# Kernel optimization log

Measured on AMD Instinct MI355X. Metric: run time of the kernel, lower is better.

Reference implementation:

```python
import jax, jax.numpy as jnp
import numpy as np

B, N, M, D, H = 2, 1024, 1024, 768, 72  # H = num_layers*nhead = 6*12

def setup_inputs() -> dict:
    key = jax.random.key(0)
    ks = jax.random.split(key, 7)
    s = lambda fan_in: 1.0 / np.sqrt(fan_in)
    return {
        "x": jax.random.normal(ks[0], (B, N, D), dtype=jnp.float32),
        "stacked_scores": jax.random.normal(ks[1], (B, H, N, M), dtype=jnp.float32),
        "W1": jax.random.uniform(ks[2], (D, D // 2), jnp.float32, -s(D), s(D)),
        "b1": jax.random.uniform(ks[3], (D // 2,), jnp.float32, -s(D), s(D)),
        "W2": jax.random.uniform(ks[4], (D // 2, H), jnp.float32, -s(D // 2), s(D // 2)),
        "b2": jax.random.uniform(ks[5], (H,), jnp.float32, -s(D // 2), s(D // 2)),
        "bias": jnp.zeros((1,), dtype=jnp.float32),
    }

def reference(x, stacked_scores, W1, b1, W2, b2, bias):
    # Router MLP: Linear -> exact GELU -> Linear  => raw_weights [b, n, h]
    h = jax.nn.gelu(jnp.einsum('bnd,df->bnf', x, W1) + b1, approximate=False)
    raw_weights = jnp.einsum('bnf,fh->bnh', h, W2) + b2
    # Weighted combine of stacked attention maps, reducing over heads
    final_matrix = jnp.einsum('bnh,bhnm->bnm', raw_weights, stacked_scores)
    return final_matrix + bias
```

## Files before the change

kernel.cpp:

```cpp
#include <hip/hip_runtime.h>
#include <math.h>

#define B_ 2
#define N_ 1024
#define M_ 1024
#define D_ 768
#define F_ 384
#define H_ 72
#define ROWS 8

typedef float f32x4 __attribute__((ext_vector_type(4)));

__global__ __launch_bounds__(512) void fused_kernel(
    const float* __restrict__ x, const float* __restrict__ scores,
    const float* __restrict__ W1, const float* __restrict__ b1,
    const float* __restrict__ W2, const float* __restrict__ b2,
    const float* __restrict__ bias, float* __restrict__ out)
{
    const int t = threadIdx.x;
    const int blk = blockIdx.x;
    const int b = blk >> 7;
    const int n0 = (blk & 127) * ROWS;
    const int row0 = (b << 10) + n0;

    __shared__ float xs[ROWS][D_];
    __shared__ float hs[ROWS][F_ + 8];
    __shared__ float rw[ROWS][80];

    {
        const f32x4* xg = reinterpret_cast<const f32x4*>(x + row0 * D_);
        f32x4* xl = reinterpret_cast<f32x4*>(&xs[0][0]);
#pragma unroll
        for (int i = 0; i < 3; ++i)
            xl[t + i * 512] = xg[t + i * 512];
    }
    __syncthreads();

    if (t < F_) {
        const int f = t;
        float acc[ROWS];
#pragma unroll
        for (int r = 0; r < ROWS; ++r) acc[r] = 0.0f;

#pragma unroll 4
        for (int d = 0; d < D_; d += 4) {
            const float w0 = W1[(d + 0) * F_ + f];
            const float w1v = W1[(d + 1) * F_ + f];
            const float w2v = W1[(d + 2) * F_ + f];
            const float w3v = W1[(d + 3) * F_ + f];
#pragma unroll
            for (int r = 0; r < ROWS; ++r) {
                const float4 xv = *reinterpret_cast<const float4*>(&xs[r][d]);
                acc[r] = fmaf(xv.x, w0, acc[r]);
                acc[r] = fmaf(xv.y, w1v, acc[r]);
                acc[r] = fmaf(xv.z, w2v, acc[r]);
                acc[r] = fmaf(xv.w, w3v, acc[r]);
            }
        }
        const float bb = b1[f];
#pragma unroll
        for (int r = 0; r < ROWS; ++r) {
            const float v = acc[r] + bb;
            hs[r][f] = 0.5f * v * (1.0f + erff(v * 0.70710678118654752f));
        }
    }
    __syncthreads();

#pragma unroll 1
    for (int o = t; o < ROWS * H_; o += 512) {
        const int r = o / H_;
        const int c = o - r * H_;
        float s = 0.0f;
#pragma unroll 4
        for (int k = 0; k < F_; k += 4) {
            const float4 hv = *reinterpret_cast<const float4*>(&hs[r][k]);
            s = fmaf(hv.x, W2[(k + 0) * H_ + c], s);
            s = fmaf(hv.y, W2[(k + 1) * H_ + c], s);
            s = fmaf(hv.z, W2[(k + 2) * H_ + c], s);
            s = fmaf(hv.w, W2[(k + 3) * H_ + c], s);
        }
        rw[r][c] = s + b2[c];
    }
    __syncthreads();

    const int col = t & 255;
    const int rp = t >> 8;
    const int r0 = rp * 4;

    const f32x4* __restrict__ sp = reinterpret_cast<const f32x4*>(scores);
    const int base = ((b * H_) * N_ + (n0 + r0)) * (M_ / 4) + col;
    const int hstr = N_ * (M_ / 4);

    f32x4 a0 = 0.f, a1 = 0.f, a2 = 0.f, a3 = 0.f;
#pragma unroll 2
    for (int h = 0; h < H_; ++h) {
        const int ib = base + h * hstr;
        const f32x4 v0 = __builtin_nontemporal_load(sp + ib);
        const f32x4 v1 = __builtin_nontemporal_load(sp + ib + 256);
        const f32x4 v2 = __builtin_nontemporal_load(sp + ib + 512);
        const f32x4 v3 = __builtin_nontemporal_load(sp + ib + 768);
        const float w0 = rw[r0 + 0][h];
        const float w1 = rw[r0 + 1][h];
        const float w2 = rw[r0 + 2][h];
        const float w3 = rw[r0 + 3][h];
#pragma unroll
        for (int j = 0; j < 4; ++j) {
            a0[j] = fmaf(w0, v0[j], a0[j]);
            a1[j] = fmaf(w1, v1[j], a1[j]);
            a2[j] = fmaf(w2, v2[j], a2[j]);
            a3[j] = fmaf(w3, v3[j], a3[j]);
        }
    }

    const float bv = bias[0];
#pragma unroll
    for (int j = 0; j < 4; ++j) { a0[j] += bv; a1[j] += bv; a2[j] += bv; a3[j] += bv; }

    f32x4* __restrict__ op = reinterpret_cast<f32x4*>(out);
    const int obase = (row0 + r0) * (M_ / 4) + col;
    __builtin_nontemporal_store(a0, op + obase);
    __builtin_nontemporal_store(a1, op + obase + 256);
    __builtin_nontemporal_store(a2, op + obase + 512);
    __builtin_nontemporal_store(a3, op + obase + 768);
}

extern "C" void kernel_launch(void* const* d_in, const int* in_sizes, int n_in,
                              void* d_out, int out_size, void* d_ws, size_t ws_size,
                              hipStream_t stream) {
    const float* x      = (const float*)d_in[0];
    const float* scores = (const float*)d_in[1];
    const float* W1     = (const float*)d_in[2];
    const float* b1     = (const float*)d_in[3];
    const float* W2     = (const float*)d_in[4];
    const float* b2     = (const float*)d_in[5];
    const float* bias   = (const float*)d_in[6];
    float* out = (float*)d_out;

    fused_kernel<<<(B_ * N_) / ROWS, 512, 0, stream>>>(
        x, scores, W1, b1, W2, b2, bias, out);
}
```

Before: 146.0 us.

## Prefetch first score heads into LDS while router MLP computes

Threads 384-511, which sat idle during the first MLP layer, now load the first three heads of stacked scores for the block's rows into a new shared-memory buffer. The combine loop then starts from head 3 out of global memory and adds the prefetched heads from LDS at the end. The aim is to overlap part of the dominant score streaming with the MLP compute. The cost is about 96KB of extra LDS per block, which likely cuts occupancy to one block per CU, and the x load is now done by only 384 threads.

New measurement: 139.3 us. 4.6% less time.

```diff
diff --git a/kernel.cpp b/kernel.cpp
--- a/kernel.cpp
+++ b/kernel.cpp
@@ -8,6 +8,7 @@
 #define F_ 384
 #define H_ 72
 #define ROWS 8
+#define PFH 3
 
 typedef float f32x4 __attribute__((ext_vector_type(4)));
 
@@ -25,18 +26,23 @@
 
     __shared__ float xs[ROWS][D_];
     __shared__ float hs[ROWS][F_ + 8];
-    __shared__ float rw[ROWS][80];
+    __shared__ float rwv[ROWS][80];
+    __shared__ float pf[PFH][ROWS][M_];
 
-    {
+    const f32x4* __restrict__ sp = reinterpret_cast<const f32x4*>(scores);
+    const int hstr = N_ * (M_ / 4);
+    const int sbase = ((b * H_) * N_ + n0) * (M_ / 4);
+
+    if (t < 384) {
         const f32x4* xg = reinterpret_cast<const f32x4*>(x + row0 * D_);
         f32x4* xl = reinterpret_cast<f32x4*>(&xs[0][0]);
 #pragma unroll
-        for (int i = 0; i < 3; ++i)
-            xl[t + i * 512] = xg[t + i * 512];
+        for (int i = 0; i < 4; ++i)
+            xl[t + i * 384] = xg[t + i * 384];
     }
     __syncthreads();
 
-    if (t < F_) {
+    if (t < 384) {
         const int f = t;
         float acc[ROWS];
 #pragma unroll
@@ -63,6 +69,23 @@
             const float v = acc[r] + bb;
             hs[r][f] = 0.5f * v * (1.0f + erff(v * 0.70710678118654752f));
         }
+    } else {
+        const int j = t - 384;
+        f32x4* pfl = reinterpret_cast<f32x4*>(&pf[0][0][0]);
+#pragma unroll 1
+        for (int base_i = 0; base_i < PFH * ROWS * 256; base_i += 128 * 12) {
+            f32x4 tmp[12];
+#pragma unroll
+            for (int u = 0; u < 12; ++u) {
+                const int i = base_i + u * 128 + j;
+                const int h = i >> 11;
+                const int rem = i & 2047;
+                tmp[u] = __builtin_nontemporal_load(sp + sbase + h * hstr + rem);
+            }
+#pragma unroll
+            for (int u = 0; u < 12; ++u)
+                pfl[base_i + u * 128 + j] = tmp[u];
+        }
     }
     __syncthreads();
 
@@ -79,30 +102,45 @@
             s = fmaf(hv.z, W2[(k + 2) * H_ + c], s);
             s = fmaf(hv.w, W2[(k + 3) * H_ + c], s);
         }
-        rw[r][c] = s + b2[c];
+        rwv[r][c] = s + b2[c];
     }
     __syncthreads();
 
     const int col = t & 255;
-    const int rp = t >> 8;
-    const int r0 = rp * 4;
+    const int r0v = (t >> 8) * 4;
 
-    const f32x4* __restrict__ sp = reinterpret_cast<const f32x4*>(scores);
-    const int base = ((b * H_) * N_ + (n0 + r0)) * (M_ / 4) + col;
-    const int hstr = N_ * (M_ / 4);
+    const int base = sbase + r0v * (M_ / 4) + col;
 
     f32x4 a0 = 0.f, a1 = 0.f, a2 = 0.f, a3 = 0.f;
 #pragma unroll 2
-    for (int h = 0; h < H_; ++h) {
+    for (int h = PFH; h < H_; ++h) {
         const int ib = base + h * hstr;
         const f32x4 v0 = __builtin_nontemporal_load(sp + ib);
         const f32x4 v1 = __builtin_nontemporal_load(sp + ib + 256);
         const f32x4 v2 = __builtin_nontemporal_load(sp + ib + 512);
         const f32x4 v3 = __builtin_nontemporal_load(sp + ib + 768);
-        const float w0 = rw[r0 + 0][h];
-        const float w1 = rw[r0 + 1][h];
-        const float w2 = rw[r0 + 2][h];
-        const float w3 = rw[r0 + 3][h];
+        const float w0 = rwv[r0v + 0][h];
+        const float w1 = rwv[r0v + 1][h];
+        const float w2 = rwv[r0v + 2][h];
+        const float w3 = rwv[r0v + 3][h];
+#pragma unroll
+        for (int j = 0; j < 4; ++j) {
+            a0[j] = fmaf(w0, v0[j], a0[j]);
+            a1[j] = fmaf(w1, v1[j], a1[j]);
+            a2[j] = fmaf(w2, v2[j], a2[j]);
+            a3[j] = fmaf(w3, v3[j], a3[j]);
+        }
+    }
+#pragma unroll
+    for (int h = 0; h < PFH; ++h) {
+        const f32x4 v0 = *reinterpret_cast<const f32x4*>(&pf[h][r0v + 0][col * 4]);
+        const f32x4 v1 = *reinterpret_cast<const f32x4*>(&pf[h][r0v + 1][col * 4]);
+        const f32x4 v2 = *reinterpret_cast<const f32x4*>(&pf[h][r0v + 2][col * 4]);
+        const f32x4 v3 = *reinterpret_cast<const f32x4*>(&pf[h][r0v + 3][col * 4]);
+        const float w0 = rwv[r0v + 0][h];
+        const float w1 = rwv[r0v + 1][h];
+        const float w2 = rwv[r0v + 2][h];
+        const float w3 = rwv[r0v + 3][h];
 #pragma unroll
         for (int j = 0; j < 4; ++j) {
             a0[j] = fmaf(w0, v0[j], a0[j]);
@@ -117,7 +155,7 @@
     for (int j = 0; j < 4; ++j) { a0[j] += bv; a1[j] += bv; a2[j] += bv; a3[j] += bv; }
 
     f32x4* __restrict__ op = reinterpret_cast<f32x4*>(out);
-    const int obase = (row0 + r0) * (M_ / 4) + col;
+    const int obase = (row0 + r0v) * (M_ / 4) + col;
     __builtin_nontemporal_store(a0, op + obase);
     __builtin_nontemporal_store(a1, op + obase + 256);
     __builtin_nontemporal_store(a2, op + obase + 512);
```
